# Optimization experiments

Measured on AMD Instinct MI355X. Metric: run time of the kernel, lower is better.

## Reference

```python
import math
import jax, jax.numpy as jnp
import numpy as np

N = 100000
F_IN = 256
H = 64
D = 16          # dim_latent
C = 8           # n_classes
L = 10          # radial_layers
K = 10          # APPNP steps
ALPHA = 0.1
BETA_PRIOR = 0.001
E = 3200000
BN_EPS = 1e-5
LOG_SCALE = 0.5 * D * math.log(4 * math.pi)


def setup_inputs() -> dict:
    key = jax.random.key(0)
    ks = jax.random.split(key, 16)
    x = jax.random.normal(ks[0], (N, F_IN), dtype=jnp.float32)
    edge_index = jax.random.randint(ks[1], (2, E), 0, N, dtype=jnp.int64)
    s1 = 1.0 / math.sqrt(F_IN)
    s2 = 1.0 / math.sqrt(H)
    return {
        'x': x,
        'edge_index': edge_index,
        'W1': jax.random.uniform(ks[2], (F_IN, H), jnp.float32, -s1, s1),
        'b1': jnp.zeros((H,), jnp.float32),
        'g1': jnp.ones((H,), jnp.float32),
        'be1': jnp.zeros((H,), jnp.float32),
        'W2': jax.random.uniform(ks[3], (H, H), jnp.float32, -s2, s2),
        'b2': jnp.zeros((H,), jnp.float32),
        'g2': jnp.ones((H,), jnp.float32),
        'be2': jnp.zeros((H,), jnp.float32),
        'W3': jax.random.uniform(ks[4], (H, D), jnp.float32, -s2, s2),
        'b3': jnp.zeros((D,), jnp.float32),
        # flow params: per layer l, per class c
        'x0': jax.random.normal(ks[5], (L, C, D), jnp.float32) * 0.1,
        'alpha_prime': jnp.zeros((L, C), jnp.float32),
        'beta_prime': jnp.zeros((L, C), jnp.float32),
        'mu': jnp.zeros((C, D), jnp.float32),
        'log_var': jnp.zeros((C, D), jnp.float32),
    }


def _batchnorm(h, g, b):
    m = h.mean(axis=0)
    v = h.var(axis=0)  # biased, as torch BN training forward
    return g * (h - m) / jnp.sqrt(v + BN_EPS) + b


def _flow_log_prob(z, x0, alpha_prime, beta_prime, mu, log_var):
    # z: [N, D] -> log q(z|c): [N, C]. Dropout off (eval); loop over L=10 layers.
    zz = jnp.broadcast_to(z[:, None, :], (z.shape[0], C, D))  # [N,C,D]
    log_det = jnp.zeros((z.shape[0], C), z.dtype)
    for l in reversed(range(L)):  # reversed(transforms)
        a = jax.nn.softplus(alpha_prime[l])[None, :, None]      # [1,C,1]
        b = -a + jax.nn.softplus(beta_prime[l])[None, :, None]
        diff = zz - x0[l][None]                                  # [N,C,D]
        r = jnp.maximum(jnp.linalg.norm(diff, axis=-1, keepdims=True), 1e-8)
        h = 1.0 / (a + r)
        zz = zz + b * h * diff
        h_prime = -1.0 / (a + r) ** 2
        log_det = log_det + (D - 1) * jnp.log1p(b * h)[..., 0] \
                  + jnp.log1p(b * h + b * h_prime * r)[..., 0]
    var = jnp.exp(log_var)  # [C,D]
    log_p_base = (-0.5 * D * math.log(2 * math.pi)
                  - 0.5 * log_var.sum(axis=-1)[None, :]
                  - 0.5 * ((zz - mu[None]) ** 2 / var[None]).sum(axis=-1))
    return log_p_base + log_det  # [N,C]


def _appnp(beta_ft, row, col, n_nodes):
    e = row.shape[0]
    deg = jax.ops.segment_sum(jnp.ones((e,), beta_ft.dtype), row, num_segments=n_nodes)
    dis = jnp.where(deg > 0, deg ** -0.5, 0.0)
    norm = dis[row] * dis[col]  # [E']
    h = beta_ft
    for _ in range(K):
        msg = jax.ops.segment_sum(norm[:, None] * h[col], row, num_segments=n_nodes)
        h = (1.0 - ALPHA) * msg + ALPHA * beta_ft
    return h


def reference(x, edge_index, W1, b1, g1, be1, W2, b2, g2, be2, W3, b3,
              x0, alpha_prime, beta_prime, mu, log_var):
    n = x.shape[0]
    # encoder (BN in batch-stats mode, dropout disabled)
    h1 = jax.nn.relu(_batchnorm(x @ W1 + b1, g1, be1))
    h2 = jax.nn.relu(_batchnorm(h1 @ W2 + b2, g2, be2))
    z = h2 @ W3 + b3  # [N,D]
    log_q = _flow_log_prob(z, x0, alpha_prime, beta_prime, mu, log_var)  # [N,C]
    beta_ft = jnp.exp(jnp.clip(log_q + LOG_SCALE, -30.0, 30.0))
    # add self loops
    sl = jnp.arange(n, dtype=edge_index.dtype)
    row = jnp.concatenate([edge_index[0], sl])
    col = jnp.concatenate([edge_index[1], sl])
    beta_agg = _appnp(beta_ft, row, col, n)
    alpha = BETA_PRIOR + jnp.maximum(beta_agg, 0.0)
    probs = alpha / alpha.sum(axis=-1, keepdims=True)
    return alpha, probs, z, beta_ft, log_q
```

## Files before the change

### kernel.cpp

```cpp
#include <hip/hip_runtime.h>

#define NFEAT_IN 256
#define HDIM 64
#define DLAT 16
#define NC 8
#define NL 10
#define KPROP 10
#define ELLW 64
#define OVF_CAP 8192
#define NB 128
#define PERTHREAD 16
#define TILE (256 * PERTHREAD)
#define BM 64
#define BK1 32

__device__ __forceinline__ float softplusf(float x) {
    return (x > 20.f) ? x : log1pf(expf(x));
}

__global__ __launch_bounds__(256) void k_gemm1(
        const float* __restrict__ x, const float* __restrict__ W1,
        const float* __restrict__ b1, float* __restrict__ t1t, int n) {
    __shared__ float xs[BM][BK1 + 4];
    __shared__ float ws[BK1][HDIM];
    int t = threadIdx.x;
    int row0 = blockIdx.x * BM;
    int tr = t >> 4, tc = t & 15;
    float acc[4][4];
    float4 bv = *reinterpret_cast<const float4*>(&b1[tc * 4]);
    #pragma unroll
    for (int i = 0; i < 4; ++i) {
        acc[i][0] = bv.x; acc[i][1] = bv.y; acc[i][2] = bv.z; acc[i][3] = bv.w;
    }
    for (int k0 = 0; k0 < NFEAT_IN; k0 += BK1) {
        __syncthreads();
        #pragma unroll
        for (int it = 0; it < 2; ++it) {
            int i = it * 256 + t;
            int row = i >> 3, q = i & 7;
            int grow = row0 + row;
            float4 v = make_float4(0.f, 0.f, 0.f, 0.f);
            if (grow < n)
                v = *reinterpret_cast<const float4*>(
                        &x[(size_t)grow * NFEAT_IN + k0 + q * 4]);
            *reinterpret_cast<float4*>(&xs[row][q * 4]) = v;
        }
        #pragma unroll
        for (int it = 0; it < 2; ++it) {
            int i = it * 256 + t;
            int kk = i >> 4, q = i & 15;
            *reinterpret_cast<float4*>(&ws[kk][q * 4]) =
                *reinterpret_cast<const float4*>(&W1[(size_t)(k0 + kk) * HDIM + q * 4]);
        }
        __syncthreads();
        #pragma unroll 8
        for (int kk = 0; kk < BK1; ++kk) {
            float a0 = xs[tr * 4 + 0][kk];
            float a1 = xs[tr * 4 + 1][kk];
            float a2 = xs[tr * 4 + 2][kk];
            float a3 = xs[tr * 4 + 3][kk];
            float4 w = *reinterpret_cast<const float4*>(&ws[kk][tc * 4]);
            acc[0][0] = fmaf(a0, w.x, acc[0][0]); acc[0][1] = fmaf(a0, w.y, acc[0][1]);
            acc[0][2] = fmaf(a0, w.z, acc[0][2]); acc[0][3] = fmaf(a0, w.w, acc[0][3]);
            acc[1][0] = fmaf(a1, w.x, acc[1][0]); acc[1][1] = fmaf(a1, w.y, acc[1][1]);
            acc[1][2] = fmaf(a1, w.z, acc[1][2]); acc[1][3] = fmaf(a1, w.w, acc[1][3]);
            acc[2][0] = fmaf(a2, w.x, acc[2][0]); acc[2][1] = fmaf(a2, w.y, acc[2][1]);
            acc[2][2] = fmaf(a2, w.z, acc[2][2]); acc[2][3] = fmaf(a2, w.w, acc[2][3]);
            acc[3][0] = fmaf(a3, w.x, acc[3][0]); acc[3][1] = fmaf(a3, w.y, acc[3][1]);
            acc[3][2] = fmaf(a3, w.z, acc[3][2]); acc[3][3] = fmaf(a3, w.w, acc[3][3]);
        }
    }
    int r = row0 + tr * 4;
    if (r < n) {
        #pragma unroll
        for (int cj = 0; cj < 4; ++cj) {
            int j = tc * 4 + cj;
            float4 v = make_float4(acc[0][cj], acc[1][cj], acc[2][cj], acc[3][cj]);
            *reinterpret_cast<float4*>(&t1t[(size_t)j * n + r]) = v;
        }
    }
}

__global__ __launch_bounds__(256) void k_gemm2(
        const float* __restrict__ t1t, const float* __restrict__ A1,
        const float* __restrict__ B1, const float* __restrict__ W2,
        const float* __restrict__ b2, float* __restrict__ t2t, int n) {
    __shared__ float xs[BK1][BM + 4];
    __shared__ float ws[BK1][HDIM];
    __shared__ float As[HDIM], Bs[HDIM];
    int t = threadIdx.x;
    int row0 = blockIdx.x * BM;
    if (t < HDIM) { As[t] = A1[t]; Bs[t] = B1[t]; }
    int tr = t >> 4, tc = t & 15;
    float acc[4][4];
    float4 bv = *reinterpret_cast<const float4*>(&b2[tc * 4]);
    #pragma unroll
    for (int i = 0; i < 4; ++i) {
        acc[i][0] = bv.x; acc[i][1] = bv.y; acc[i][2] = bv.z; acc[i][3] = bv.w;
    }
    for (int k0 = 0; k0 < HDIM; k0 += BK1) {
        __syncthreads();
        #pragma unroll
        for (int it = 0; it < 2; ++it) {
            int i = it * 256 + t;
            int kk = i >> 4, q = i & 15;
            float4 v = make_float4(0.f, 0.f, 0.f, 0.f);
            if (row0 + q * 4 < n) {
                v = *reinterpret_cast<const float4*>(
                        &t1t[(size_t)(k0 + kk) * n + row0 + q * 4]);
                float a = As[k0 + kk], b = Bs[k0 + kk];
                v.x = fmaxf(fmaf(a, v.x, b), 0.f);
                v.y = fmaxf(fmaf(a, v.y, b), 0.f);
                v.z = fmaxf(fmaf(a, v.z, b), 0.f);
                v.w = fmaxf(fmaf(a, v.w, b), 0.f);
            }
            *reinterpret_cast<float4*>(&xs[kk][q * 4]) = v;
        }
        #pragma unroll
        for (int it = 0; it < 2; ++it) {
            int i = it * 256 + t;
            int kk = i >> 4, q = i & 15;
            *reinterpret_cast<float4*>(&ws[kk][q * 4]) =
                *reinterpret_cast<const float4*>(&W2[(size_t)(k0 + kk) * HDIM + q * 4]);
        }
        __syncthreads();
        #pragma unroll 8
        for (int kk = 0; kk < BK1; ++kk) {
            float4 a = *reinterpret_cast<const float4*>(&xs[kk][tr * 4]);
            float4 w = *reinterpret_cast<const float4*>(&ws[kk][tc * 4]);
            acc[0][0] = fmaf(a.x, w.x, acc[0][0]); acc[0][1] = fmaf(a.x, w.y, acc[0][1]);
            acc[0][2] = fmaf(a.x, w.z, acc[0][2]); acc[0][3] = fmaf(a.x, w.w, acc[0][3]);
            acc[1][0] = fmaf(a.y, w.x, acc[1][0]); acc[1][1] = fmaf(a.y, w.y, acc[1][1]);
            acc[1][2] = fmaf(a.y, w.z, acc[1][2]); acc[1][3] = fmaf(a.y, w.w, acc[1][3]);
            acc[2][0] = fmaf(a.z, w.x, acc[2][0]); acc[2][1] = fmaf(a.z, w.y, acc[2][1]);
            acc[2][2] = fmaf(a.z, w.z, acc[2][2]); acc[2][3] = fmaf(a.z, w.w, acc[2][3]);
            acc[3][0] = fmaf(a.w, w.x, acc[3][0]); acc[3][1] = fmaf(a.w, w.y, acc[3][1]);
            acc[3][2] = fmaf(a.w, w.z, acc[3][2]); acc[3][3] = fmaf(a.w, w.w, acc[3][3]);
        }
    }
    int r = row0 + tr * 4;
    if (r < n) {
        #pragma unroll
        for (int cj = 0; cj < 4; ++cj) {
            int j = tc * 4 + cj;
            float4 v = make_float4(acc[0][cj], acc[1][cj], acc[2][cj], acc[3][cj]);
            *reinterpret_cast<float4*>(&t2t[(size_t)j * n + r]) = v;
        }
    }
}

__global__ __launch_bounds__(256) void k_stats(
        const float* __restrict__ tt, float* __restrict__ sum,
        float* __restrict__ sq, int n) {
    int feat = blockIdx.x >> 3;
    int chunk = blockIdx.x & 7;
    const float4* p = reinterpret_cast<const float4*>(tt + (size_t)feat * n);
    int n4 = n / 4;
    float s = 0.f, q = 0.f;
    for (int i = chunk * 256 + threadIdx.x; i < n4; i += 8 * 256) {
        float4 v = p[i];
        s += v.x + v.y + v.z + v.w;
        q += v.x * v.x + v.y * v.y + v.z * v.z + v.w * v.w;
    }
    if (chunk == 0 && threadIdx.x < (n & 3)) {
        float v = tt[(size_t)feat * n + (n & ~3) + threadIdx.x];
        s += v; q += v * v;
    }
    #pragma unroll
    for (int off = 32; off; off >>= 1) {
        s += __shfl_down(s, off, 64);
        q += __shfl_down(q, off, 64);
    }
    __shared__ float ls[4], lq[4];
    int wid = threadIdx.x >> 6, lane = threadIdx.x & 63;
    if (lane == 0) { ls[wid] = s; lq[wid] = q; }
    __syncthreads();
    if (threadIdx.x == 0) {
        atomicAdd(&sum[feat], ls[0] + ls[1] + ls[2] + ls[3]);
        atomicAdd(&sq[feat],  lq[0] + lq[1] + lq[2] + lq[3]);
    }
}

__global__ void k_finalize(const float* __restrict__ sum, const float* __restrict__ sq,
        const float* __restrict__ g, const float* __restrict__ be,
        float* __restrict__ A, float* __restrict__ B, int n) {
    int j = threadIdx.x;
    if (j >= HDIM) return;
    float mean = sum[j] / (float)n;
    float var = sq[j] / (float)n - mean * mean;
    float istd = 1.0f / sqrtf(var + 1e-5f);
    A[j] = g[j] * istd;
    B[j] = be[j] - mean * istd * g[j];
}

__global__ __launch_bounds__(256) void k_zlin(
        const float* __restrict__ t2t, const float* __restrict__ A2,
        const float* __restrict__ B2, const float* __restrict__ W3,
        const float* __restrict__ b3, float* __restrict__ out_z, int n) {
    __shared__ float As[HDIM], Bs[HDIM], Ws[HDIM * DLAT];
    int t = threadIdx.x;
    if (t < HDIM) { As[t] = A2[t]; Bs[t] = B2[t]; }
    for (int i = t; i < HDIM * DLAT; i += 256) Ws[i] = W3[i];
    __syncthreads();
    int row = blockIdx.x * 256 + t;
    if (row >= n) return;
    float z[DLAT];
    #pragma unroll
    for (int j = 0; j < DLAT; ++j) z[j] = b3[j];
    for (int k = 0; k < HDIM; ++k) {
        float hv = fmaxf(fmaf(As[k], t2t[(size_t)k * n + row], Bs[k]), 0.f);
        const float* w = &Ws[k * DLAT];
        #pragma unroll
        for (int j = 0; j < DLAT; ++j) z[j] = fmaf(hv, w[j], z[j]);
    }
    float4* zp = reinterpret_cast<float4*>(&out_z[(size_t)row * DLAT]);
    zp[0] = make_float4(z[0], z[1], z[2], z[3]);
    zp[1] = make_float4(z[4], z[5], z[6], z[7]);
    zp[2] = make_float4(z[8], z[9], z[10], z[11]);
    zp[3] = make_float4(z[12], z[13], z[14], z[15]);
}

__global__ __launch_bounds__(256) void k_flow(
        const float* __restrict__ zbuf, const float* __restrict__ x0,
        const float* __restrict__ ap, const float* __restrict__ bp,
        const float* __restrict__ mu, const float* __restrict__ lv,
        float* __restrict__ out_logq, float* __restrict__ out_beta, int n) {
    __shared__ float a_s[NL * NC], b_s[NL * NC];
    __shared__ float x0_s[NL * NC][DLAT + 1];
    __shared__ float mu_s[NC][DLAT + 1], iv_s[NC][DLAT + 1], slv_s[NC];
    int t = threadIdx.x;
    for (int i = t; i < NL * NC; i += 256) {
        float a = softplusf(ap[i]);
        a_s[i] = a;
        b_s[i] = softplusf(bp[i]) - a;
    }
    for (int i = t; i < NL * NC * DLAT; i += 256) x0_s[i >> 4][i & 15] = x0[i];
    for (int i = t; i < NC * DLAT; i += 256) {
        mu_s[i >> 4][i & 15] = mu[i];
        iv_s[i >> 4][i & 15] = __expf(-lv[i]);
    }
    if (t < NC) {
        float s = 0.f;
        for (int d = 0; d < DLAT; ++d) s += lv[t * DLAT + d];
        slv_s[t] = s;
    }
    __syncthreads();
    int gid = blockIdx.x * 256 + t;
    int row = gid >> 3, c = gid & 7;
    if (row >= n) return;
    float zz[DLAT];
    const float4* zp = reinterpret_cast<const float4*>(&zbuf[(size_t)row * DLAT]);
    float4 z0 = zp[0], z1 = zp[1], z2 = zp[2], z3 = zp[3];
    zz[0] = z0.x; zz[1] = z0.y; zz[2] = z0.z; zz[3] = z0.w;
    zz[4] = z1.x; zz[5] = z1.y; zz[6] = z1.z; zz[7] = z1.w;
    zz[8] = z2.x; zz[9] = z2.y; zz[10] = z2.z; zz[11] = z2.w;
    zz[12] = z3.x; zz[13] = z3.y; zz[14] = z3.z; zz[15] = z3.w;

    float log_det = 0.f;
    #pragma unroll
    for (int l = NL - 1; l >= 0; --l) {
        int idx = l * NC + c;
        float a = a_s[idx], b = b_s[idx];
        const float* x0p = x0_s[idx];
        float diff[DLAT];
        float r2 = 0.f;
        #pragma unroll
        for (int d = 0; d < DLAT; ++d) {
            diff[d] = zz[d] - x0p[d];
            r2 = fmaf(diff[d], diff[d], r2);
        }
        float r = fmaxf(sqrtf(r2), 1e-8f);
        float h = 1.f / (a + r);
        float bh = b * h;
        #pragma unroll
        for (int d = 0; d < DLAT; ++d) zz[d] = fmaf(bh, diff[d], zz[d]);
        log_det += (DLAT - 1) * __logf(1.f + bh) + __logf(1.f + bh - bh * h * r);
    }
    float quad = 0.f;
    #pragma unroll
    for (int d = 0; d < DLAT; ++d) {
        float dd = zz[d] - mu_s[c][d];
        quad = fmaf(dd * dd, iv_s[c][d], quad);
    }
    float lq = -14.70301653f - 0.5f * slv_s[c] - 0.5f * quad + log_det;
    out_logq[gid] = lq;
    float w = fminf(fmaxf(lq + 20.24819398f, -30.f), 30.f);
    out_beta[gid] = __expf(w);
}

__global__ __launch_bounds__(256) void k_bucket(
        const int* __restrict__ rows, const int* __restrict__ cols,
        int2* __restrict__ bpairs, int* __restrict__ bcnt, int cap,
        int* __restrict__ cur, int2* __restrict__ ovf, int* __restrict__ ovf_cnt,
        int e, int n, int rpb) {
    __shared__ int lcnt[NB], loff[NB], lcur[NB], gbase[NB], sc[NB];
    __shared__ int2 staged[TILE];
    int t = threadIdx.x;
    int base = blockIdx.x * TILE;
    for (int i = t; i < NB; i += 256) lcnt[i] = 0;
    __syncthreads();
    int er[PERTHREAD], ec[PERTHREAD], eb[PERTHREAD];
    #pragma unroll
    for (int k = 0; k < PERTHREAD; ++k) {
        int i = base + k * 256 + t;
        eb[k] = -1;
        if (i < e) {
            int r = rows[i], c = cols[i];
            if ((unsigned)r < (unsigned)n && (unsigned)c < (unsigned)n) {
                er[k] = r; ec[k] = c;
                int b = (int)((unsigned)r / (unsigned)rpb);
                eb[k] = b;
                atomicAdd(&lcnt[b], 1);
            }
        }
    }
    __syncthreads();
    if (t < NB) sc[t] = lcnt[t];
    __syncthreads();
    for (int off = 1; off < NB; off <<= 1) {
        int v = 0;
        if (t < NB && t >= off) v = sc[t - off];
        __syncthreads();
        if (t < NB) sc[t] += v;
        __syncthreads();
    }
    if (t < NB) { loff[t] = sc[t] - lcnt[t]; lcur[t] = sc[t] - lcnt[t]; }
    __syncthreads();
    #pragma unroll
    for (int k = 0; k < PERTHREAD; ++k) {
        if (eb[k] >= 0) {
            int slot = atomicAdd(&lcur[eb[k]], 1);
            staged[slot] = make_int2(er[k], ec[k]);
        }
    }
    __syncthreads();
    if (t < NB && lcnt[t] > 0) gbase[t] = atomicAdd(&bcnt[t], lcnt[t]);
    __syncthreads();
    int wid = t >> 6, lane = t & 63;
    for (int b = wid; b < NB; b += 4) {
        int cnt = lcnt[b];
        if (!cnt) continue;
        int gb = gbase[b], lo = loff[b];
        for (int k = lane; k < cnt; k += 64) {
            int2 p = staged[lo + k];
            int dst = gb + k;
            if (dst < cap) {
                bpairs[(size_t)b * cap + dst] = p;
            } else {
                int o = atomicAdd(ovf_cnt, 1);
                if (o < OVF_CAP) ovf[o] = p;
                atomicAdd(&cur[p.x], 1);
            }
        }
    }
}

__global__ __launch_bounds__(256) void k_build(
        const int2* __restrict__ bpairs, const int* __restrict__ bcnt, int cap,
        int* __restrict__ ecol, int* __restrict__ cur,
        int2* __restrict__ ovf, int* __restrict__ ovf_cnt, int n, int rpb) {
    __shared__ int lcnt[1024];
    int b = blockIdx.x, t = threadIdx.x;
    int row_base = b * rpb;
    int nrows = n - row_base; if (nrows > rpb) nrows = rpb;
    if (nrows <= 0) return;
    for (int i = t; i < nrows; i += 256) lcnt[i] = 0;
    __syncthreads();
    int m = bcnt[b]; if (m > cap) m = cap;
    const int2* bp = bpairs + (size_t)b * cap;
    for (int i = t; i < m; i += 256) {
        int2 p = bp[i];
        int lr = p.x - row_base;
        int j = atomicAdd(&lcnt[lr], 1);
        if (j < ELLW) {
            ecol[(size_t)p.x * ELLW + j] = p.y;
        } else {
            int o = atomicAdd(ovf_cnt, 1);
            if (o < OVF_CAP) ovf[o] = p;
        }
    }
    __syncthreads();
    for (int i = t; i < nrows; i += 256) {
        int c = lcnt[i];
        if (c) cur[row_base + i] += c;
    }
}

__global__ void k_dis(const int* __restrict__ cur, float* __restrict__ dis, int n) {
    int i = blockIdx.x * blockDim.x + threadIdx.x;
    if (i < n) dis[i] = rsqrtf((float)cur[i] + 1.0f);
}

__global__ void k_init_hs(const float* __restrict__ beta, const float* __restrict__ dis,
                          float* __restrict__ hs, int n) {
    int i = blockIdx.x * blockDim.x + threadIdx.x;
    if (i >= n) return;
    float d = dis[i];
    const float4* b = reinterpret_cast<const float4*>(beta + (size_t)i * NC);
    float4* o = reinterpret_cast<float4*>(hs + (size_t)i * NC);
    float4 b0 = b[0], b1 = b[1];
    o[0] = make_float4(d * b0.x, d * b0.y, d * b0.z, d * b0.w);
    o[1] = make_float4(d * b1.x, d * b1.y, d * b1.z, d * b1.w);
}

__global__ __launch_bounds__(256) void k_gather(
        const int* __restrict__ cur, const int* __restrict__ ecol,
        const float* __restrict__ hs_in, const float* __restrict__ beta,
        const float* __restrict__ dis, float* __restrict__ hout,
        float* __restrict__ hs_out, const int2* __restrict__ ovf,
        const int* __restrict__ ovf_cnt, int n) {
    int row = (blockIdx.x * blockDim.x + threadIdx.x) >> 3;
    int c = threadIdx.x & 7;
    if (row >= n) return;
    int cnt = cur[row];
    int lim = cnt < ELLW ? cnt : ELLW;
    float d = dis[row];
    const int* ec = ecol + (size_t)row * ELLW;
    const int4* ec4 = reinterpret_cast<const int4*>(ec);
    float acc = hs_in[row * NC + c];
    float s0 = 0.f, s1 = 0.f, s2 = 0.f, s3 = 0.f;
    float s4 = 0.f, s5 = 0.f, s6 = 0.f, s7 = 0.f;
    int lim8 = lim & ~7;
    for (int ep = 0; ep < lim8; ep += 8) {
        int4 e0 = ec4[(ep >> 2) + 0];
        int4 e1 = ec4[(ep >> 2) + 1];
        s0 += hs_in[e0.x * NC + c];
        s1 += hs_in[e0.y * NC + c];
        s2 += hs_in[e0.z * NC + c];
        s3 += hs_in[e0.w * NC + c];
        s4 += hs_in[e1.x * NC + c];
        s5 += hs_in[e1.y * NC + c];
        s6 += hs_in[e1.z * NC + c];
        s7 += hs_in[e1.w * NC + c];
    }
    for (int ep = lim8; ep < lim; ++ep) acc += hs_in[ec[ep] * NC + c];
    acc += ((s0 + s1) + (s2 + s3)) + ((s4 + s5) + (s6 + s7));
    int m = *ovf_cnt;
    if (m > 0) {
        if (m > OVF_CAP) m = OVF_CAP;
        for (int i = 0; i < m; ++i) {
            int2 p = ovf[i];
            if (p.x == row) acc += hs_in[p.y * NC + c];
        }
    }
    float hn = 0.9f * d * acc + 0.1f * beta[row * NC + c];
    hout[row * NC + c] = hn;
    hs_out[row * NC + c] = d * hn;
}

__global__ void k_final(const float* __restrict__ h, float* __restrict__ out_alpha,
        float* __restrict__ out_probs, int n) {
    int i = blockIdx.x * blockDim.x + threadIdx.x;
    if (i >= n) return;
    float a[NC];
    float s = 0.f;
    #pragma unroll
    for (int c = 0; c < NC; ++c) {
        float v = h[(size_t)i * NC + c];
        v = 0.001f + fmaxf(v, 0.f);
        a[c] = v; s += v;
    }
    float inv = 1.f / s;
    #pragma unroll
    for (int c = 0; c < NC; ++c) {
        out_alpha[(size_t)i * NC + c] = a[c];
        out_probs[(size_t)i * NC + c] = a[c] * inv;
    }
}

extern "C" void kernel_launch(void* const* d_in, const int* in_sizes, int n_in,
                              void* d_out, int out_size, void* d_ws, size_t ws_size,
                              hipStream_t stream) {
    const float* x   = (const float*)d_in[0];
    const int*   ei  = (const int*)d_in[1];
    const float* W1  = (const float*)d_in[2];
    const float* b1  = (const float*)d_in[3];
    const float* g1  = (const float*)d_in[4];
    const float* be1 = (const float*)d_in[5];
    const float* W2  = (const float*)d_in[6];
    const float* b2  = (const float*)d_in[7];
    const float* g2  = (const float*)d_in[8];
    const float* be2 = (const float*)d_in[9];
    const float* W3  = (const float*)d_in[10];
    const float* b3  = (const float*)d_in[11];
    const float* x0  = (const float*)d_in[12];
    const float* ap  = (const float*)d_in[13];
    const float* bp  = (const float*)d_in[14];
    const float* mu  = (const float*)d_in[15];
    const float* lv  = (const float*)d_in[16];

    int n = in_sizes[0] / NFEAT_IN;
    int e = in_sizes[1] / 2;
    const int* rows = ei;
    const int* cols = ei + e;
    int rpb = (n + NB - 1) / NB;
    int cap = (e + e / 16) / NB;

    size_t an = (size_t)HDIM * n;
    float* ws  = (float*)d_ws;
    float* t1t = ws;
    float* t2t = ws + an;
    int2*  bpairs = (int2*)t2t;
    float* stats = (float*)((char*)t2t + (size_t)NB * cap * sizeof(int2));
    float *sum1 = stats,       *sq1 = stats + 64,  *A1 = stats + 128, *B1 = stats + 192;
    float *sum2 = stats + 256, *sq2 = stats + 320, *A2 = stats + 384, *B2 = stats + 448;
    int*  bcnt    = (int*)(stats + 512);
    int*  ovf_cnt = bcnt + NB;
    int2* ovf     = (int2*)(ovf_cnt + 4);
    float* hs0 = (float*)bpairs;
    float* hs1 = hs0 + (size_t)NC * n;
    int* ecol = (int*)t1t;

    float* out = (float*)d_out;
    float* out_alpha = out;
    float* out_probs = out + (size_t)n * NC;
    float* out_z     = out + (size_t)2 * n * NC;
    float* out_beta  = out_z + (size_t)n * DLAT;
    float* out_logq  = out_beta + (size_t)n * NC;

    int*   cur = (int*)out_probs;
    float* dis = out_probs + n;

    int nb_nodes = (n + 255) / 256;
    int nb_gemm  = (n + BM - 1) / BM;
    int nb_nc    = (int)(((size_t)n * NC + 255) / 256);

    hipMemsetAsync(stats, 0, (512 + NB + 4) * sizeof(float), stream);

    k_gemm1<<<nb_gemm, 256, 0, stream>>>(x, W1, b1, t1t, n);
    k_stats<<<HDIM * 8, 256, 0, stream>>>(t1t, sum1, sq1, n);
    k_finalize<<<1, 64, 0, stream>>>(sum1, sq1, g1, be1, A1, B1, n);
    k_gemm2<<<nb_gemm, 256, 0, stream>>>(t1t, A1, B1, W2, b2, t2t, n);
    k_stats<<<HDIM * 8, 256, 0, stream>>>(t2t, sum2, sq2, n);
    k_finalize<<<1, 64, 0, stream>>>(sum2, sq2, g2, be2, A2, B2, n);
    k_zlin<<<nb_nodes, 256, 0, stream>>>(t2t, A2, B2, W3, b3, out_z, n);
    k_flow<<<nb_nc, 256, 0, stream>>>(out_z, x0, ap, bp, mu, lv,
                                      out_logq, out_beta, n);

    hipMemsetAsync(cur, 0, (size_t)n * sizeof(int), stream);
    int nt_bucket = (e + TILE - 1) / TILE;
    k_bucket<<<nt_bucket, 256, 0, stream>>>(rows, cols, bpairs, bcnt, cap,
                                            cur, ovf, ovf_cnt, e, n, rpb);
    k_build<<<NB, 256, 0, stream>>>(bpairs, bcnt, cap, ecol, cur, ovf, ovf_cnt, n, rpb);
    k_dis<<<nb_nodes, 256, 0, stream>>>(cur, dis, n);
    k_init_hs<<<nb_nodes, 256, 0, stream>>>(out_beta, dis, hs0, n);

    for (int it = 0; it < KPROP; ++it) {
        const float* hin = (it & 1) ? hs1 : hs0;
        float* hso = (it & 1) ? hs0 : hs1;
        k_gather<<<nb_nc, 256, 0, stream>>>(cur, ecol, hin, out_beta, dis,
                                            out_alpha, hso, ovf, ovf_cnt, n);
    }
    k_final<<<nb_nodes, 256, 0, stream>>>(out_alpha, out_alpha, out_probs, n);
}
```

Baseline: 518.9 us.

## Fuse BatchNorm statistics into GEMM epilogues and drop redundant propagation stores

The per-feature sum and sum-of-squares for both BatchNorm layers are now computed from each GEMM's accumulators in registers, reduced across the block with wave shuffles and shared memory, and added atomically. This removes the two separate k_stats passes that re-read the full 64×N intermediates. The gather kernel no longer writes an unscaled copy of h on every propagation step; the final kernel rebuilds it from the scaled state by dividing by dis. gemm1's inner loop now reads A from shared memory as float4. The cost is extra shared memory and a few block-level atomics per GEMM block, and the last h is recovered through a division.

```diff
diff --git a/kernel.cpp b/kernel.cpp
--- a/kernel.cpp
+++ b/kernel.cpp
@@ -18,11 +18,51 @@
     return (x > 20.f) ? x : log1pf(expf(x));
 }
 
+__device__ __forceinline__ void fma16(float a0, float a1, float a2, float a3,
+                                      const float4 wv, float acc[4][4]) {
+    acc[0][0] = fmaf(a0, wv.x, acc[0][0]); acc[0][1] = fmaf(a0, wv.y, acc[0][1]);
+    acc[0][2] = fmaf(a0, wv.z, acc[0][2]); acc[0][3] = fmaf(a0, wv.w, acc[0][3]);
+    acc[1][0] = fmaf(a1, wv.x, acc[1][0]); acc[1][1] = fmaf(a1, wv.y, acc[1][1]);
+    acc[1][2] = fmaf(a1, wv.z, acc[1][2]); acc[1][3] = fmaf(a1, wv.w, acc[1][3]);
+    acc[2][0] = fmaf(a2, wv.x, acc[2][0]); acc[2][1] = fmaf(a2, wv.y, acc[2][1]);
+    acc[2][2] = fmaf(a2, wv.z, acc[2][2]); acc[2][3] = fmaf(a2, wv.w, acc[2][3]);
+    acc[3][0] = fmaf(a3, wv.x, acc[3][0]); acc[3][1] = fmaf(a3, wv.y, acc[3][1]);
+    acc[3][2] = fmaf(a3, wv.z, acc[3][2]); acc[3][3] = fmaf(a3, wv.w, acc[3][3]);
+}
+
+__device__ __forceinline__ void stats_epilogue(
+        float s[4], float q[4], int t, float (*swr)[64], float (*sqr)[64],
+        float* __restrict__ sum, float* __restrict__ sq) {
+    #pragma unroll
+    for (int off = 16; off < 64; off <<= 1) {
+        #pragma unroll
+        for (int cj = 0; cj < 4; ++cj) {
+            s[cj] += __shfl_xor(s[cj], off, 64);
+            q[cj] += __shfl_xor(q[cj], off, 64);
+        }
+    }
+    int wid = t >> 6, lane = t & 63;
+    if (lane < 16) {
+        #pragma unroll
+        for (int cj = 0; cj < 4; ++cj) {
+            swr[wid][lane * 4 + cj] = s[cj];
+            sqr[wid][lane * 4 + cj] = q[cj];
+        }
+    }
+    __syncthreads();
+    if (t < 64) {
+        atomicAdd(&sum[t], swr[0][t] + swr[1][t] + swr[2][t] + swr[3][t]);
+        atomicAdd(&sq[t],  sqr[0][t] + sqr[1][t] + sqr[2][t] + sqr[3][t]);
+    }
+}
+
 __global__ __launch_bounds__(256) void k_gemm1(
         const float* __restrict__ x, const float* __restrict__ W1,
-        const float* __restrict__ b1, float* __restrict__ t1t, int n) {
+        const float* __restrict__ b1, float* __restrict__ t1t,
+        float* __restrict__ sum1, float* __restrict__ sq1, int n) {
     __shared__ float xs[BM][BK1 + 4];
     __shared__ float ws[BK1][HDIM];
+    __shared__ float swr[4][64], sqr[4][64];
     int t = threadIdx.x;
     int row0 = blockIdx.x * BM;
     int tr = t >> 4, tc = t & 15;
@@ -37,37 +77,36 @@
         #pragma unroll
         for (int it = 0; it < 2; ++it) {
             int i = it * 256 + t;
-            int row = i >> 3, q = i & 7;
+            int row = i >> 3, qq = i & 7;
             int grow = row0 + row;
             float4 v = make_float4(0.f, 0.f, 0.f, 0.f);
             if (grow < n)
                 v = *reinterpret_cast<const float4*>(
-                        &x[(size_t)grow * NFEAT_IN + k0 + q * 4]);
-            *reinterpret_cast<float4*>(&xs[row][q * 4]) = v;
+                        &x[(size_t)grow * NFEAT_IN + k0 + qq * 4]);
+            *reinterpret_cast<float4*>(&xs[row][qq * 4]) = v;
         }
         #pragma unroll
         for (int it = 0; it < 2; ++it) {
             int i = it * 256 + t;
-            int kk = i >> 4, q = i & 15;
-            *reinterpret_cast<float4*>(&ws[kk][q * 4]) =
-                *reinterpret_cast<const float4*>(&W1[(size_t)(k0 + kk) * HDIM + q * 4]);
+            int kk = i >> 4, qq = i & 15;
+            *reinterpret_cast<float4*>(&ws[kk][qq * 4]) =
+                *reinterpret_cast<const float4*>(&W1[(size_t)(k0 + kk) * HDIM + qq * 4]);
         }
         __syncthreads();
-        #pragma unroll 8
-        for (int kk = 0; kk < BK1; ++kk) {
-            float a0 = xs[tr * 4 + 0][kk];
-            float a1 = xs[tr * 4 + 1][kk];
-            float a2 = xs[tr * 4 + 2][kk];
-            float a3 = xs[tr * 4 + 3][kk];
-            float4 w = *reinterpret_cast<const float4*>(&ws[kk][tc * 4]);
-            acc[0][0] = fmaf(a0, w.x, acc[0][0]); acc[0][1] = fmaf(a0, w.y, acc[0][1]);
-            acc[0][2] = fmaf(a0, w.z, acc[0][2]); acc[0][3] = fmaf(a0, w.w, acc[0][3]);
-            acc[1][0] = fmaf(a1, w.x, acc[1][0]); acc[1][1] = fmaf(a1, w.y, acc[1][1]);
-            acc[1][2] = fmaf(a1, w.z, acc[1][2]); acc[1][3] = fmaf(a1, w.w, acc[1][3]);
-            acc[2][0] = fmaf(a2, w.x, acc[2][0]); acc[2][1] = fmaf(a2, w.y, acc[2][1]);
-            acc[2][2] = fmaf(a2, w.z, acc[2][2]); acc[2][3] = fmaf(a2, w.w, acc[2][3]);
-            acc[3][0] = fmaf(a3, w.x, acc[3][0]); acc[3][1] = fmaf(a3, w.y, acc[3][1]);
-            acc[3][2] = fmaf(a3, w.z, acc[3][2]); acc[3][3] = fmaf(a3, w.w, acc[3][3]);
+        #pragma unroll
+        for (int kq = 0; kq < BK1 / 4; ++kq) {
+            float4 a0 = *reinterpret_cast<const float4*>(&xs[tr * 4 + 0][kq * 4]);
+            float4 a1 = *reinterpret_cast<const float4*>(&xs[tr * 4 + 1][kq * 4]);
+            float4 a2 = *reinterpret_cast<const float4*>(&xs[tr * 4 + 2][kq * 4]);
+            float4 a3 = *reinterpret_cast<const float4*>(&xs[tr * 4 + 3][kq * 4]);
+            float4 w0 = *reinterpret_cast<const float4*>(&ws[kq * 4 + 0][tc * 4]);
+            float4 w1 = *reinterpret_cast<const float4*>(&ws[kq * 4 + 1][tc * 4]);
+            float4 w2 = *reinterpret_cast<const float4*>(&ws[kq * 4 + 2][tc * 4]);
+            float4 w3 = *reinterpret_cast<const float4*>(&ws[kq * 4 + 3][tc * 4]);
+            fma16(a0.x, a1.x, a2.x, a3.x, w0, acc);
+            fma16(a0.y, a1.y, a2.y, a3.y, w1, acc);
+            fma16(a0.z, a1.z, a2.z, a3.z, w2, acc);
+            fma16(a0.w, a1.w, a2.w, a3.w, w3, acc);
         }
     }
     int r = row0 + tr * 4;
@@ -79,15 +118,30 @@
             *reinterpret_cast<float4*>(&t1t[(size_t)j * n + r]) = v;
         }
     }
+    float s[4] = {0.f, 0.f, 0.f, 0.f}, q[4] = {0.f, 0.f, 0.f, 0.f};
+    #pragma unroll
+    for (int i = 0; i < 4; ++i) {
+        if (row0 + tr * 4 + i < n) {
+            #pragma unroll
+            for (int cj = 0; cj < 4; ++cj) {
+                float v = acc[i][cj];
+                s[cj] += v; q[cj] += v * v;
+            }
+        }
+    }
+    __syncthreads();
+    stats_epilogue(s, q, t, swr, sqr, sum1, sq1);
 }
 
 __global__ __launch_bounds__(256) void k_gemm2(
         const float* __restrict__ t1t, const float* __restrict__ A1,
         const float* __restrict__ B1, const float* __restrict__ W2,
-        const float* __restrict__ b2, float* __restrict__ t2t, int n) {
+        const float* __restrict__ b2, float* __restrict__ t2t,
+        float* __restrict__ sum2, float* __restrict__ sq2, int n) {
     __shared__ float xs[BK1][BM + 4];
     __shared__ float ws[BK1][HDIM];
     __shared__ float As[HDIM], Bs[HDIM];
+    __shared__ float swr[4][64], sqr[4][64];
     int t = threadIdx.x;
     int row0 = blockIdx.x * BM;
     if (t < HDIM) { As[t] = A1[t]; Bs[t] = B1[t]; }
@@ -103,39 +157,32 @@
         #pragma unroll
         for (int it = 0; it < 2; ++it) {
             int i = it * 256 + t;
-            int kk = i >> 4, q = i & 15;
+            int kk = i >> 4, qq = i & 15;
             float4 v = make_float4(0.f, 0.f, 0.f, 0.f);
-            if (row0 + q * 4 < n) {
+            if (row0 + qq * 4 < n) {
                 v = *reinterpret_cast<const float4*>(
-                        &t1t[(size_t)(k0 + kk) * n + row0 + q * 4]);
+                        &t1t[(size_t)(k0 + kk) * n + row0 + qq * 4]);
                 float a = As[k0 + kk], b = Bs[k0 + kk];
                 v.x = fmaxf(fmaf(a, v.x, b), 0.f);
                 v.y = fmaxf(fmaf(a, v.y, b), 0.f);
                 v.z = fmaxf(fmaf(a, v.z, b), 0.f);
                 v.w = fmaxf(fmaf(a, v.w, b), 0.f);
             }
-            *reinterpret_cast<float4*>(&xs[kk][q * 4]) = v;
+            *reinterpret_cast<float4*>(&xs[kk][qq * 4]) = v;
         }
         #pragma unroll
         for (int it = 0; it < 2; ++it) {
             int i = it * 256 + t;
-            int kk = i >> 4, q = i & 15;
-            *reinterpret_cast<float4*>(&ws[kk][q * 4]) =
-                *reinterpret_cast<const float4*>(&W2[(size_t)(k0 + kk) * HDIM + q * 4]);
+            int kk = i >> 4, qq = i & 15;
+            *reinterpret_cast<float4*>(&ws[kk][qq * 4]) =
+                *reinterpret_cast<const float4*>(&W2[(size_t)(k0 + kk) * HDIM + qq * 4]);
         }
         __syncthreads();
         #pragma unroll 8
         for (int kk = 0; kk < BK1; ++kk) {
             float4 a = *reinterpret_cast<const float4*>(&xs[kk][tr * 4]);
             float4 w = *reinterpret_cast<const float4*>(&ws[kk][tc * 4]);
-            acc[0][0] = fmaf(a.x, w.x, acc[0][0]); acc[0][1] = fmaf(a.x, w.y, acc[0][1]);
-            acc[0][2] = fmaf(a.x, w.z, acc[0][2]); acc[0][3] = fmaf(a.x, w.w, acc[0][3]);
-            acc[1][0] = fmaf(a.y, w.x, acc[1][0]); acc[1][1] = fmaf(a.y, w.y, acc[1][1]);
-            acc[1][2] = fmaf(a.y, w.z, acc[1][2]); acc[1][3] = fmaf(a.y, w.w, acc[1][3]);
-            acc[2][0] = fmaf(a.z, w.x, acc[2][0]); acc[2][1] = fmaf(a.z, w.y, acc[2][1]);
-            acc[2][2] = fmaf(a.z, w.z, acc[2][2]); acc[2][3] = fmaf(a.z, w.w, acc[2][3]);
-            acc[3][0] = fmaf(a.w, w.x, acc[3][0]); acc[3][1] = fmaf(a.w, w.y, acc[3][1]);
-            acc[3][2] = fmaf(a.w, w.z, acc[3][2]); acc[3][3] = fmaf(a.w, w.w, acc[3][3]);
+            fma16(a.x, a.y, a.z, a.w, w, acc);
         }
     }
     int r = row0 + tr * 4;
@@ -147,38 +194,19 @@
             *reinterpret_cast<float4*>(&t2t[(size_t)j * n + r]) = v;
         }
     }
-}
-
-__global__ __launch_bounds__(256) void k_stats(
-        const float* __restrict__ tt, float* __restrict__ sum,
-        float* __restrict__ sq, int n) {
-    int feat = blockIdx.x >> 3;
-    int chunk = blockIdx.x & 7;
-    const float4* p = reinterpret_cast<const float4*>(tt + (size_t)feat * n);
-    int n4 = n / 4;
-    float s = 0.f, q = 0.f;
-    for (int i = chunk * 256 + threadIdx.x; i < n4; i += 8 * 256) {
-        float4 v = p[i];
-        s += v.x + v.y + v.z + v.w;
-        q += v.x * v.x + v.y * v.y + v.z * v.z + v.w * v.w;
-    }
-    if (chunk == 0 && threadIdx.x < (n & 3)) {
-        float v = tt[(size_t)feat * n + (n & ~3) + threadIdx.x];
-        s += v; q += v * v;
-    }
-    #pragma unroll
-    for (int off = 32; off; off >>= 1) {
-        s += __shfl_down(s, off, 64);
-        q += __shfl_down(q, off, 64);
-    }
-    __shared__ float ls[4], lq[4];
-    int wid = threadIdx.x >> 6, lane = threadIdx.x & 63;
-    if (lane == 0) { ls[wid] = s; lq[wid] = q; }
-    __syncthreads();
-    if (threadIdx.x == 0) {
-        atomicAdd(&sum[feat], ls[0] + ls[1] + ls[2] + ls[3]);
-        atomicAdd(&sq[feat],  lq[0] + lq[1] + lq[2] + lq[3]);
-    }
+    float s[4] = {0.f, 0.f, 0.f, 0.f}, q[4] = {0.f, 0.f, 0.f, 0.f};
+    #pragma unroll
+    for (int i = 0; i < 4; ++i) {
+        if (row0 + tr * 4 + i < n) {
+            #pragma unroll
+            for (int cj = 0; cj < 4; ++cj) {
+                float v = acc[i][cj];
+                s[cj] += v; q[cj] += v * v;
+            }
+        }
+    }
+    __syncthreads();
+    stats_epilogue(s, q, t, swr, sqr, sum2, sq2);
 }
 
 __global__ void k_finalize(const float* __restrict__ sum, const float* __restrict__ sq,
@@ -406,9 +434,8 @@
 __global__ __launch_bounds__(256) void k_gather(
         const int* __restrict__ cur, const int* __restrict__ ecol,
         const float* __restrict__ hs_in, const float* __restrict__ beta,
-        const float* __restrict__ dis, float* __restrict__ hout,
-        float* __restrict__ hs_out, const int2* __restrict__ ovf,
-        const int* __restrict__ ovf_cnt, int n) {
+        const float* __restrict__ dis, float* __restrict__ hs_out,
+        const int2* __restrict__ ovf, const int* __restrict__ ovf_cnt, int n) {
     int row = (blockIdx.x * blockDim.x + threadIdx.x) >> 3;
     int c = threadIdx.x & 7;
     if (row >= n) return;
@@ -444,19 +471,19 @@
         }
     }
     float hn = 0.9f * d * acc + 0.1f * beta[row * NC + c];
-    hout[row * NC + c] = hn;
     hs_out[row * NC + c] = d * hn;
 }
 
-__global__ void k_final(const float* __restrict__ h, float* __restrict__ out_alpha,
-        float* __restrict__ out_probs, int n) {
+__global__ void k_final(const float* __restrict__ hs, const float* __restrict__ dis,
+        float* __restrict__ out_alpha, float* __restrict__ out_probs, int n) {
     int i = blockIdx.x * blockDim.x + threadIdx.x;
     if (i >= n) return;
+    float inv_d = 1.f / dis[i];
     float a[NC];
     float s = 0.f;
     #pragma unroll
     for (int c = 0; c < NC; ++c) {
-        float v = h[(size_t)i * NC + c];
+        float v = hs[(size_t)i * NC + c] * inv_d;
         v = 0.001f + fmaxf(v, 0.f);
         a[c] = v; s += v;
     }
@@ -507,6 +534,8 @@
     int*  bcnt    = (int*)(stats + 512);
     int*  ovf_cnt = bcnt + NB;
     int2* ovf     = (int2*)(ovf_cnt + 4);
+    int*   cur = (int*)(ovf + OVF_CAP);
+    float* dis = (float*)(cur + n);
     float* hs0 = (float*)bpairs;
     float* hs1 = hs0 + (size_t)NC * n;
     int* ecol = (int*)t1t;
@@ -518,26 +547,21 @@
     float* out_beta  = out_z + (size_t)n * DLAT;
     float* out_logq  = out_beta + (size_t)n * NC;
 
-    int*   cur = (int*)out_probs;
-    float* dis = out_probs + n;
-
     int nb_nodes = (n + 255) / 256;
     int nb_gemm  = (n + BM - 1) / BM;
     int nb_nc    = (int)(((size_t)n * NC + 255) / 256);
 
-    hipMemsetAsync(stats, 0, (512 + NB + 4) * sizeof(float), stream);
-
-    k_gemm1<<<nb_gemm, 256, 0, stream>>>(x, W1, b1, t1t, n);
-    k_stats<<<HDIM * 8, 256, 0, stream>>>(t1t, sum1, sq1, n);
+    (void)hipMemsetAsync(stats, 0, (512 + NB + 4) * sizeof(float), stream);
+
+    k_gemm1<<<nb_gemm, 256, 0, stream>>>(x, W1, b1, t1t, sum1, sq1, n);
     k_finalize<<<1, 64, 0, stream>>>(sum1, sq1, g1, be1, A1, B1, n);
-    k_gemm2<<<nb_gemm, 256, 0, stream>>>(t1t, A1, B1, W2, b2, t2t, n);
-    k_stats<<<HDIM * 8, 256, 0, stream>>>(t2t, sum2, sq2, n);
+    k_gemm2<<<nb_gemm, 256, 0, stream>>>(t1t, A1, B1, W2, b2, t2t, sum2, sq2, n);
     k_finalize<<<1, 64, 0, stream>>>(sum2, sq2, g2, be2, A2, B2, n);
     k_zlin<<<nb_nodes, 256, 0, stream>>>(t2t, A2, B2, W3, b3, out_z, n);
     k_flow<<<nb_nc, 256, 0, stream>>>(out_z, x0, ap, bp, mu, lv,
                                       out_logq, out_beta, n);
 
-    hipMemsetAsync(cur, 0, (size_t)n * sizeof(int), stream);
+    (void)hipMemsetAsync(cur, 0, (size_t)n * sizeof(int), stream);
     int nt_bucket = (e + TILE - 1) / TILE;
     k_bucket<<<nt_bucket, 256, 0, stream>>>(rows, cols, bpairs, bcnt, cap,
                                             cur, ovf, ovf_cnt, e, n, rpb);
@@ -549,7 +573,7 @@
         const float* hin = (it & 1) ? hs1 : hs0;
         float* hso = (it & 1) ? hs0 : hs1;
         k_gather<<<nb_nc, 256, 0, stream>>>(cur, ecol, hin, out_beta, dis,
-                                            out_alpha, hso, ovf, ovf_cnt, n);
-    }
-    k_final<<<nb_nodes, 256, 0, stream>>>(out_alpha, out_alpha, out_probs, n);
-}
+                                            hso, ovf, ovf_cnt, n);
+    }
+    k_final<<<nb_nodes, 256, 0, stream>>>(hs0, dis, out_alpha, out_probs, n);
+}
```

After: 539.3 us. +3.9%, slower.
